# Performance work log

Measured on AMD Instinct MI355X. Metric: run time of the kernel, lower is better.

The kernel has to match this reference:

```python
import jax, jax.numpy as jnp
import numpy as np

QUANT_LEVELS = jnp.array([-1.5, -0.5, 0.5, 1.5], dtype=jnp.float32)
EPS = 1e-5


def setup_inputs() -> dict:
    key = jax.random.key(0)
    k1, k2, k3 = jax.random.split(key, 3)
    B, S, D_IN, D_OUT = 4, 2048, 4096, 4096
    x = jax.random.normal(k1, (B, S, D_IN), dtype=jnp.float32)
    weight_2bit = jax.random.randint(k2, (D_OUT, D_IN), 0, 4, dtype=jnp.int32)
    weight_scale = jnp.ones((1,), dtype=jnp.float32)
    bias = jax.random.normal(k3, (D_OUT,), dtype=jnp.float32)
    return {"x": x, "weight_2bit": weight_2bit, "weight_scale": weight_scale, "bias": bias}


def reference(x, weight_2bit, weight_scale, bias):
    # per-row (last-dim) absmax activation normalization
    x_abs_max = jnp.clip(jnp.max(jnp.abs(x), axis=-1, keepdims=True), EPS)  # [B,S,1]
    x_norm = x / x_abs_max
    # dequantize 2-bit codes to {-1.5,-0.5,0.5,1.5}
    weight_float = QUANT_LEVELS[weight_2bit]  # [D_out, D_in]
    # F.linear: x_norm @ W^T
    out = jnp.einsum('bsd,od->bso', x_norm, weight_float)
    out = out * (x_abs_max * weight_scale)
    out = out + bias
    return out
```

## Files before the change

### kernel.cpp

```cpp
#include <hip/hip_runtime.h>
#include <hip/hip_bf16.h>

typedef __attribute__((ext_vector_type(4))) int i32x4;

#define GLOAD16(gp, lp)                                                        \
  __builtin_amdgcn_global_load_lds(                                            \
      (const __attribute__((address_space(1))) unsigned int*)(const void*)(gp),\
      (__attribute__((address_space(3))) unsigned int*)(void*)(lp), 16, 0, 0)

#define LGKM(n) asm volatile("s_waitcnt lgkmcnt(" #n ")" ::: "memory")
#define VMCNT(n) asm volatile("s_waitcnt vmcnt(" #n ")" ::: "memory")
#define BAR() __builtin_amdgcn_s_barrier()


__global__ void quant_x_i8(const float* __restrict__ x,
                           signed char* __restrict__ xq,
                           float* __restrict__ amax, int K) {
  const int row = blockIdx.x;
  const float* xr = x + (long)row * K;
  const int tid = threadIdx.x;
  const int nv4 = K >> 2;
  float m = 0.f;
  for (int j = tid; j < nv4; j += blockDim.x) {
    float4 v = ((const float4*)xr)[j];
    m = fmaxf(m, fmaxf(fmaxf(fabsf(v.x), fabsf(v.y)),
                       fmaxf(fabsf(v.z), fabsf(v.w))));
  }
  for (int off = 32; off; off >>= 1) m = fmaxf(m, __shfl_xor(m, off));
  __shared__ float red[16];
  const int wid = tid >> 6, lane = tid & 63;
  const int nw = blockDim.x >> 6;
  if (lane == 0) red[wid] = m;
  __syncthreads();
  m = red[0];
  for (int w = 1; w < nw; ++w) m = fmaxf(m, red[w]);
  m = fmaxf(m, 1e-5f);
  if (tid == 0) amax[row] = m;
  const float s = 127.0f / m;
  signed char* xqr = xq + (long)row * K;
  for (int j = tid; j < nv4; j += blockDim.x) {
    float4 v = ((const float4*)xr)[j];
    union { signed char c[4]; int i; } u;
    u.c[0] = (signed char)__float2int_rn(v.x * s);
    u.c[1] = (signed char)__float2int_rn(v.y * s);
    u.c[2] = (signed char)__float2int_rn(v.z * s);
    u.c[3] = (signed char)__float2int_rn(v.w * s);
    ((int*)xqr)[j] = u.i;
  }
}

__global__ void cvt_w_i8(const int* __restrict__ codes,
                         signed char* __restrict__ w8, long n16) {
  long stride = (long)gridDim.x * blockDim.x;
  for (long i = (long)blockIdx.x * blockDim.x + threadIdx.x; i < n16; i += stride) {
    const int4* p = (const int4*)(codes + i * 16);
    int4 a = p[0], b = p[1], c = p[2], d = p[3];
    union { signed char ch[16]; int4 v; } u;
    u.ch[0] = (signed char)(2 * a.x - 3);  u.ch[1] = (signed char)(2 * a.y - 3);
    u.ch[2] = (signed char)(2 * a.z - 3);  u.ch[3] = (signed char)(2 * a.w - 3);
    u.ch[4] = (signed char)(2 * b.x - 3);  u.ch[5] = (signed char)(2 * b.y - 3);
    u.ch[6] = (signed char)(2 * b.z - 3);  u.ch[7] = (signed char)(2 * b.w - 3);
    u.ch[8] = (signed char)(2 * c.x - 3);  u.ch[9] = (signed char)(2 * c.y - 3);
    u.ch[10] = (signed char)(2 * c.z - 3); u.ch[11] = (signed char)(2 * c.w - 3);
    u.ch[12] = (signed char)(2 * d.x - 3); u.ch[13] = (signed char)(2 * d.y - 3);
    u.ch[14] = (signed char)(2 * d.z - 3); u.ch[15] = (signed char)(2 * d.w - 3);
    *(int4*)(w8 + i * 16) = u.v;
  }
}


template <int MIH>
__device__ __forceinline__ void rdA8(const signed char* Asb, i32x4 (&a)[4][2],
                                     int arow, int ccol) {
#pragma unroll
  for (int m4 = 0; m4 < 4; ++m4)
#pragma unroll
    for (int kk = 0; kk < 2; ++kk)
      a[m4][kk] = *(const i32x4*)(Asb + MIH * 16384 + m4 * 2048 + arow +
                                  (ccol ^ (kk << 6)));
}

template <int NIH>
__device__ __forceinline__ void rdB8(const signed char* Bsb, i32x4 (&b)[4][2],
                                     int brw, int ccol) {
#pragma unroll
  for (int n2 = 0; n2 < 2; ++n2)
#pragma unroll
    for (int kk = 0; kk < 2; ++kk)
      b[NIH * 2 + n2][kk] = *(const i32x4*)(Bsb + NIH * 16384 + n2 * 2048 +
                                            brw + (ccol ^ (kk << 6)));
}

template <int MH, int NH>
__device__ __forceinline__ void quad8(i32x4 (&acc)[8][4], const i32x4 (&a)[4][2],
                                      const i32x4 (&b)[4][2]) {
#pragma unroll
  for (int m4 = 0; m4 < 4; ++m4)
#pragma unroll
    for (int n2 = 0; n2 < 2; ++n2)
#pragma unroll
      for (int kk = 0; kk < 2; ++kk)
        acc[MH * 4 + m4][NH * 2 + n2] = __builtin_amdgcn_mfma_i32_16x16x64_i8(
            a[m4][kk], b[NH * 2 + n2][kk], acc[MH * 4 + m4][NH * 2 + n2], 0, 0, 0);
}

__global__ void __launch_bounds__(512, 2) gemm256_i8(
    const signed char* __restrict__ A, const signed char* __restrict__ B,
    const float* __restrict__ amax, const float* __restrict__ bias,
    const float* __restrict__ scalep, float* __restrict__ C, int M, int N,
    int K) {
  extern __shared__ signed char lds[];
  signed char* As0 = lds;
  signed char* As1 = lds + 32768;
  signed char* Bs0 = lds + 65536;
  signed char* Bs1 = lds + 98304;

  const int tid = threadIdx.x;
  const int lane = tid & 63;
  const int wid = tid >> 6;
  const int wr = wid >> 2;
  const int wc = wid & 3;
  const int l15 = lane & 15;
  const int l7 = lane & 7;
  const int lq = lane >> 4;

  const int NT = K >> 7;
  const int nbx = N >> 8;
  const int nwg = gridDim.x;
  const int bid = blockIdx.x;
  const int swz = ((nwg & 7) == 0) ? ((bid & 7) * (nwg >> 3) + (bid >> 3)) : bid;
  const int bx = swz % nbx;
  const int by = swz / nbx;
  const long brow = (long)by << 8;
  const long bcol = (long)bx << 8;

  const signed char* Ag = A + brow * K;
  const signed char* Bg = B + bcol * K;

  const int srl0 = tid >> 3;
  const int scol = ((lane & 7) ^ (lane >> 3)) << 4;
  const int ccol = (lq ^ l7) << 4;
  const int arow = wr * 8192 + l15 * 128;
  const int brw = wc * 4096 + l15 * 128;

  auto stA = [&](signed char* dst, int h, int kt) {
    if (kt >= NT) return;
    const long k0 = ((long)kt << 7) + scol;
#pragma unroll
    for (int r = 0; r < 2; ++r) {
      const int srl = srl0 + (r << 6);
      const int ar = ((srl >> 6) << 7) + (h << 6) + (srl & 63);
      GLOAD16(Ag + (long)ar * K + k0, dst + (h << 14) + (r << 13) + (wid << 10));
    }
  };
  auto stB = [&](signed char* dst, int h, int kt) {
    if (kt >= NT) return;
    const long k0 = ((long)kt << 7) + scol;
#pragma unroll
    for (int r = 0; r < 2; ++r) {
      const int srl = srl0 + (r << 6);
      const int br = ((srl >> 5) << 6) + (((h << 1) + ((srl >> 4) & 1)) << 4) +
                     (srl & 15);
      GLOAD16(Bg + (long)br * K + k0, dst + (h << 14) + (r << 13) + (wid << 10));
    }
  };

  stA(As0, 0, 0); stB(Bs0, 0, 0); stB(Bs0, 1, 0); stA(As0, 1, 0);
  stA(As1, 0, 1); stB(Bs1, 0, 1); stB(Bs1, 1, 1);
  VMCNT(6);
  BAR();

  i32x4 a[4][2], b[4][2];
  i32x4 acc[8][4] = {};

  const int NI = NT >> 1;
  for (int i = 0; i < NI; ++i) {
    const int T = i << 1;
    rdA8<0>(As0, a, arow, ccol);
    rdB8<0>(Bs0, b, brw, ccol);
    stA(As1, 1, T + 1);
    LGKM(8);
    BAR(); LGKM(0);
    __builtin_amdgcn_s_setprio(1); quad8<0, 0>(acc, a, b); __builtin_amdgcn_s_setprio(0);
    BAR();
    rdB8<1>(Bs0, b, brw, ccol);
    stA(As0, 0, T + 2);
    BAR(); LGKM(0);
    __builtin_amdgcn_s_setprio(1); quad8<0, 1>(acc, a, b); __builtin_amdgcn_s_setprio(0);
    BAR();
    rdA8<1>(As0, a, arow, ccol);
    stB(Bs0, 0, T + 2);
    BAR(); LGKM(0);
    __builtin_amdgcn_s_setprio(1); quad8<1, 0>(acc, a, b); __builtin_amdgcn_s_setprio(0);
    BAR();
    stB(Bs0, 1, T + 2);
    BAR();
    __builtin_amdgcn_s_setprio(1); quad8<1, 1>(acc, a, b); __builtin_amdgcn_s_setprio(0);
    if (T + 4 <= NT) { VMCNT(6); } else { VMCNT(0); }
    BAR();
    rdA8<0>(As1, a, arow, ccol);
    rdB8<0>(Bs1, b, brw, ccol);
    stA(As0, 1, T + 2);
    LGKM(8);
    BAR(); LGKM(0);
    __builtin_amdgcn_s_setprio(1); quad8<0, 0>(acc, a, b); __builtin_amdgcn_s_setprio(0);
    BAR();
    rdB8<1>(Bs1, b, brw, ccol);
    stA(As1, 0, T + 3);
    BAR(); LGKM(0);
    __builtin_amdgcn_s_setprio(1); quad8<0, 1>(acc, a, b); __builtin_amdgcn_s_setprio(0);
    BAR();
    rdA8<1>(As1, a, arow, ccol);
    stB(Bs1, 0, T + 3);
    BAR(); LGKM(0);
    __builtin_amdgcn_s_setprio(1); quad8<1, 0>(acc, a, b); __builtin_amdgcn_s_setprio(0);
    BAR();
    stB(Bs1, 1, T + 3);
    BAR();
    __builtin_amdgcn_s_setprio(1); quad8<1, 1>(acc, a, b); __builtin_amdgcn_s_setprio(0);
    if (i + 1 < NI) { VMCNT(6); } else { VMCNT(0); }
    BAR();
  }

  const float ws = scalep[0] * (1.0f / 254.0f);
#pragma unroll
  for (int mi = 0; mi < 8; ++mi) {
    const long row0 = brow + wr * 128 + mi * 16 + lq * 4;
    float am[4];
#pragma unroll
    for (int r = 0; r < 4; ++r) am[r] = amax[row0 + r] * ws;
#pragma unroll
    for (int ni = 0; ni < 4; ++ni) {
      const long col = bcol + wc * 64 + ni * 16 + l15;
      const float bv = bias[col];
#pragma unroll
      for (int r = 0; r < 4; ++r)
        C[(row0 + r) * (long)N + col] = (float)acc[mi][ni][r] * am[r] + bv;
    }
  }
}


__global__ void naive_gemm(const float* __restrict__ x, const int* __restrict__ w2,
                           const float* __restrict__ scalep,
                           const float* __restrict__ bias, float* __restrict__ out,
                           long M, int N, int K) {
  long idx = (long)blockIdx.x * blockDim.x + threadIdx.x;
  if (idx >= M * (long)N) return;
  long m = idx / N;
  int n = (int)(idx % N);
  const float* xr = x + m * (long)K;
  const int* wr = w2 + (long)n * K;
  float s = 0.f;
  for (int k = 0; k < K; ++k) s += xr[k] * ((float)wr[k] - 1.5f);
  out[idx] = s * scalep[0] + bias[n];
}


extern "C" void kernel_launch(void* const* d_in, const int* in_sizes, int n_in,
                              void* d_out, int out_size, void* d_ws, size_t ws_size,
                              hipStream_t stream) {
  const float* x = (const float*)d_in[0];
  const int* w2 = (const int*)d_in[1];
  const float* wscale = (const float*)d_in[2];
  const float* bias = (const float*)d_in[3];
  float* out = (float*)d_out;

  const long xn = (long)in_sizes[0];
  const long wn = (long)in_sizes[1];
  const int N = in_sizes[3];
  const int K = (int)(wn / N);
  const long M = xn / K;

  const size_t need = (size_t)xn + (size_t)wn + (size_t)M * 4;
  const bool fast = (ws_size >= need) && (M % 256 == 0) && (N % 256 == 0) &&
                    (K % 128 == 0) && (wn % 16 == 0);

  if (fast) {
    signed char* xq = (signed char*)d_ws;
    signed char* w8 = (signed char*)d_ws + xn;
    float* amax = (float*)((signed char*)d_ws + xn + wn);

    quant_x_i8<<<(int)M, 256, 0, stream>>>(x, xq, amax, K);
    cvt_w_i8<<<2048, 256, 0, stream>>>(w2, w8, wn / 16);

    hipFuncSetAttribute((const void*)gemm256_i8,
                        hipFuncAttributeMaxDynamicSharedMemorySize, 131072);
    const int grid = (int)((M / 256) * (N / 256));
    gemm256_i8<<<grid, 512, 131072, stream>>>(xq, w8, amax, bias, wscale, out,
                                              (int)M, N, K);
  } else {
    const long total = M * (long)N;
    const int blocks = (int)((total + 255) / 256);
    naive_gemm<<<blocks, 256, 0, stream>>>(x, w2, wscale, bias, out, M, N, K);
  }
}
```

Before: 187.3 us.

## Switch int8 GEMM to 32x32x32 MFMA and merge prep kernels

Replaces the 16x16x64 int8 MFMA tiling with 32x32x32 int8 MFMA instructions. This changes the LDS read pattern, the accumulator layout (i32x16) and the epilogue row mapping. It also merges the activation-quantize and weight-convert kernels into one launch, split by block index. The larger MFMA tiles are meant to cut LDS reads per MAC and raise matrix-core efficiency, while the merged prep removes one launch and lets the two prep jobs run concurrently. The risks are the different throughput of the new instruction and possible LDS bank conflicts from the new read swizzle.

```diff
diff --git a/kernel.cpp b/kernel.cpp
--- a/kernel.cpp
+++ b/kernel.cpp
@@ -2,6 +2,7 @@
 #include <hip/hip_bf16.h>
 
 typedef __attribute__((ext_vector_type(4))) int i32x4;
+typedef __attribute__((ext_vector_type(16))) int i32x16;
 
 #define GLOAD16(gp, lp)                                                        \
   __builtin_amdgcn_global_load_lds(                                            \
@@ -13,95 +14,94 @@
 #define BAR() __builtin_amdgcn_s_barrier()
 
 
-__global__ void quant_x_i8(const float* __restrict__ x,
-                           signed char* __restrict__ xq,
-                           float* __restrict__ amax, int K) {
-  const int row = blockIdx.x;
-  const float* xr = x + (long)row * K;
+__global__ void prep_i8(const float* __restrict__ x,
+                        const int* __restrict__ codes,
+                        signed char* __restrict__ xq,
+                        signed char* __restrict__ w8,
+                        float* __restrict__ amax, int K, int M, long n16) {
+  __shared__ float red[16];
   const int tid = threadIdx.x;
-  const int nv4 = K >> 2;
-  float m = 0.f;
-  for (int j = tid; j < nv4; j += blockDim.x) {
-    float4 v = ((const float4*)xr)[j];
-    m = fmaxf(m, fmaxf(fmaxf(fabsf(v.x), fabsf(v.y)),
-                       fmaxf(fabsf(v.z), fabsf(v.w))));
+  if ((int)blockIdx.x < M) {
+    const int row = blockIdx.x;
+    const float* xr = x + (long)row * K;
+    const int nv4 = K >> 2;
+    float m = 0.f;
+    for (int j = tid; j < nv4; j += blockDim.x) {
+      float4 v = ((const float4*)xr)[j];
+      m = fmaxf(m, fmaxf(fmaxf(fabsf(v.x), fabsf(v.y)),
+                         fmaxf(fabsf(v.z), fabsf(v.w))));
+    }
+    for (int off = 32; off; off >>= 1) m = fmaxf(m, __shfl_xor(m, off));
+    const int wid = tid >> 6, lane = tid & 63;
+    const int nw = blockDim.x >> 6;
+    if (lane == 0) red[wid] = m;
+    __syncthreads();
+    m = red[0];
+    for (int w = 1; w < nw; ++w) m = fmaxf(m, red[w]);
+    m = fmaxf(m, 1e-5f);
+    if (tid == 0) amax[row] = m;
+    const float s = 127.0f / m;
+    signed char* xqr = xq + (long)row * K;
+    for (int j = tid; j < nv4; j += blockDim.x) {
+      float4 v = ((const float4*)xr)[j];
+      union { signed char c[4]; int i; } u;
+      u.c[0] = (signed char)__float2int_rn(v.x * s);
+      u.c[1] = (signed char)__float2int_rn(v.y * s);
+      u.c[2] = (signed char)__float2int_rn(v.z * s);
+      u.c[3] = (signed char)__float2int_rn(v.w * s);
+      ((int*)xqr)[j] = u.i;
+    }
+  } else {
+    const long stride = (long)(gridDim.x - M) * blockDim.x;
+    for (long i = (long)(blockIdx.x - M) * blockDim.x + tid; i < n16;
+         i += stride) {
+      const int4* p = (const int4*)(codes + i * 16);
+      int4 a = p[0], b = p[1], c = p[2], d = p[3];
+      union { signed char ch[16]; int4 v; } u;
+      u.ch[0] = (signed char)(2 * a.x - 3);  u.ch[1] = (signed char)(2 * a.y - 3);
+      u.ch[2] = (signed char)(2 * a.z - 3);  u.ch[3] = (signed char)(2 * a.w - 3);
+      u.ch[4] = (signed char)(2 * b.x - 3);  u.ch[5] = (signed char)(2 * b.y - 3);
+      u.ch[6] = (signed char)(2 * b.z - 3);  u.ch[7] = (signed char)(2 * b.w - 3);
+      u.ch[8] = (signed char)(2 * c.x - 3);  u.ch[9] = (signed char)(2 * c.y - 3);
+      u.ch[10] = (signed char)(2 * c.z - 3); u.ch[11] = (signed char)(2 * c.w - 3);
+      u.ch[12] = (signed char)(2 * d.x - 3); u.ch[13] = (signed char)(2 * d.y - 3);
+      u.ch[14] = (signed char)(2 * d.z - 3); u.ch[15] = (signed char)(2 * d.w - 3);
+      *(int4*)(w8 + i * 16) = u.v;
+    }
   }
-  for (int off = 32; off; off >>= 1) m = fmaxf(m, __shfl_xor(m, off));
-  __shared__ float red[16];
-  const int wid = tid >> 6, lane = tid & 63;
-  const int nw = blockDim.x >> 6;
-  if (lane == 0) red[wid] = m;
-  __syncthreads();
-  m = red[0];
-  for (int w = 1; w < nw; ++w) m = fmaxf(m, red[w]);
-  m = fmaxf(m, 1e-5f);
-  if (tid == 0) amax[row] = m;
-  const float s = 127.0f / m;
-  signed char* xqr = xq + (long)row * K;
-  for (int j = tid; j < nv4; j += blockDim.x) {
-    float4 v = ((const float4*)xr)[j];
-    union { signed char c[4]; int i; } u;
-    u.c[0] = (signed char)__float2int_rn(v.x * s);
-    u.c[1] = (signed char)__float2int_rn(v.y * s);
-    u.c[2] = (signed char)__float2int_rn(v.z * s);
-    u.c[3] = (signed char)__float2int_rn(v.w * s);
-    ((int*)xqr)[j] = u.i;
-  }
-}
-
-__global__ void cvt_w_i8(const int* __restrict__ codes,
-                         signed char* __restrict__ w8, long n16) {
-  long stride = (long)gridDim.x * blockDim.x;
-  for (long i = (long)blockIdx.x * blockDim.x + threadIdx.x; i < n16; i += stride) {
-    const int4* p = (const int4*)(codes + i * 16);
-    int4 a = p[0], b = p[1], c = p[2], d = p[3];
-    union { signed char ch[16]; int4 v; } u;
-    u.ch[0] = (signed char)(2 * a.x - 3);  u.ch[1] = (signed char)(2 * a.y - 3);
-    u.ch[2] = (signed char)(2 * a.z - 3);  u.ch[3] = (signed char)(2 * a.w - 3);
-    u.ch[4] = (signed char)(2 * b.x - 3);  u.ch[5] = (signed char)(2 * b.y - 3);
-    u.ch[6] = (signed char)(2 * b.z - 3);  u.ch[7] = (signed char)(2 * b.w - 3);
-    u.ch[8] = (signed char)(2 * c.x - 3);  u.ch[9] = (signed char)(2 * c.y - 3);
-    u.ch[10] = (signed char)(2 * c.z - 3); u.ch[11] = (signed char)(2 * c.w - 3);
-    u.ch[12] = (signed char)(2 * d.x - 3); u.ch[13] = (signed char)(2 * d.y - 3);
-    u.ch[14] = (signed char)(2 * d.z - 3); u.ch[15] = (signed char)(2 * d.w - 3);
-    *(int4*)(w8 + i * 16) = u.v;
-  }
-}
-
-
-template <int MIH>
-__device__ __forceinline__ void rdA8(const signed char* Asb, i32x4 (&a)[4][2],
-                                     int arow, int ccol) {
-#pragma unroll
-  for (int m4 = 0; m4 < 4; ++m4)
-#pragma unroll
-    for (int kk = 0; kk < 2; ++kk)
-      a[m4][kk] = *(const i32x4*)(Asb + MIH * 16384 + m4 * 2048 + arow +
-                                  (ccol ^ (kk << 6)));
-}
-
-template <int NIH>
-__device__ __forceinline__ void rdB8(const signed char* Bsb, i32x4 (&b)[4][2],
-                                     int brw, int ccol) {
-#pragma unroll
-  for (int n2 = 0; n2 < 2; ++n2)
-#pragma unroll
-    for (int kk = 0; kk < 2; ++kk)
-      b[NIH * 2 + n2][kk] = *(const i32x4*)(Bsb + NIH * 16384 + n2 * 2048 +
-                                            brw + (ccol ^ (kk << 6)));
-}
-
-template <int MH, int NH>
-__device__ __forceinline__ void quad8(i32x4 (&acc)[8][4], const i32x4 (&a)[4][2],
-                                      const i32x4 (&b)[4][2]) {
-#pragma unroll
-  for (int m4 = 0; m4 < 4; ++m4)
-#pragma unroll
-    for (int n2 = 0; n2 < 2; ++n2)
-#pragma unroll
-      for (int kk = 0; kk < 2; ++kk)
-        acc[MH * 4 + m4][NH * 2 + n2] = __builtin_amdgcn_mfma_i32_16x16x64_i8(
-            a[m4][kk], b[NH * 2 + n2][kk], acc[MH * 4 + m4][NH * 2 + n2], 0, 0, 0);
+}
+
+
+template <int MH>
+__device__ __forceinline__ void rdA32(const signed char* Asb, i32x4 (&a)[2][4],
+                                      int abase, int c0) {
+#pragma unroll
+  for (int mb2 = 0; mb2 < 2; ++mb2)
+#pragma unroll
+    for (int kk = 0; kk < 4; ++kk)
+      a[mb2][kk] = *(const i32x4*)(Asb + MH * 16384 + abase + mb2 * 4096 +
+                                   ((((kk << 1) ^ c0)) << 4));
+}
+
+template <int NB>
+__device__ __forceinline__ void rdB32(const signed char* Bsb, i32x4 (&b)[2][4],
+                                      int bbase, int c0) {
+#pragma unroll
+  for (int kk = 0; kk < 4; ++kk)
+    b[NB][kk] = *(const i32x4*)(Bsb + NB * 16384 + bbase +
+                                ((((kk << 1) ^ c0)) << 4));
+}
+
+template <int MH, int NB>
+__device__ __forceinline__ void quad32(i32x16 (&acc)[4][2],
+                                       const i32x4 (&a)[2][4],
+                                       const i32x4 (&b)[2][4]) {
+#pragma unroll
+  for (int mb2 = 0; mb2 < 2; ++mb2)
+#pragma unroll
+    for (int kk = 0; kk < 4; ++kk)
+      acc[MH * 2 + mb2][NB] = __builtin_amdgcn_mfma_i32_32x32x32_i8(
+          a[mb2][kk], b[NB][kk], acc[MH * 2 + mb2][NB], 0, 0, 0);
 }
 
 __global__ void __launch_bounds__(512, 2) gemm256_i8(
@@ -120,9 +120,9 @@
   const int wid = tid >> 6;
   const int wr = wid >> 2;
   const int wc = wid & 3;
-  const int l15 = lane & 15;
+  const int l31 = lane & 31;
   const int l7 = lane & 7;
-  const int lq = lane >> 4;
+  const int lhi = lane >> 5;
 
   const int NT = K >> 7;
   const int nbx = N >> 8;
@@ -139,9 +139,9 @@
 
   const int srl0 = tid >> 3;
   const int scol = ((lane & 7) ^ (lane >> 3)) << 4;
-  const int ccol = (lq ^ l7) << 4;
-  const int arow = wr * 8192 + l15 * 128;
-  const int brw = wc * 4096 + l15 * 128;
+  const int c0 = lhi ^ l7;
+  const int abase = (wr * 64 + l31) * 128;
+  const int bbase = (wc * 32 + l31) * 128;
 
   auto stA = [&](signed char* dst, int h, int kt) {
     if (kt >= NT) return;
@@ -170,72 +170,75 @@
   VMCNT(6);
   BAR();
 
-  i32x4 a[4][2], b[4][2];
-  i32x4 acc[8][4] = {};
+  i32x4 a[2][4], b[2][4];
+  i32x16 acc[4][2] = {};
 
   const int NI = NT >> 1;
   for (int i = 0; i < NI; ++i) {
     const int T = i << 1;
-    rdA8<0>(As0, a, arow, ccol);
-    rdB8<0>(Bs0, b, brw, ccol);
+    rdA32<0>(As0, a, abase, c0);
+    rdB32<0>(Bs0, b, bbase, c0);
     stA(As1, 1, T + 1);
     LGKM(8);
     BAR(); LGKM(0);
-    __builtin_amdgcn_s_setprio(1); quad8<0, 0>(acc, a, b); __builtin_amdgcn_s_setprio(0);
-    BAR();
-    rdB8<1>(Bs0, b, brw, ccol);
+    __builtin_amdgcn_s_setprio(1); quad32<0, 0>(acc, a, b); __builtin_amdgcn_s_setprio(0);
+    BAR();
+    rdB32<1>(Bs0, b, bbase, c0);
     stA(As0, 0, T + 2);
     BAR(); LGKM(0);
-    __builtin_amdgcn_s_setprio(1); quad8<0, 1>(acc, a, b); __builtin_amdgcn_s_setprio(0);
-    BAR();
-    rdA8<1>(As0, a, arow, ccol);
+    __builtin_amdgcn_s_setprio(1); quad32<0, 1>(acc, a, b); __builtin_amdgcn_s_setprio(0);
+    BAR();
+    rdA32<1>(As0, a, abase, c0);
     stB(Bs0, 0, T + 2);
     BAR(); LGKM(0);
-    __builtin_amdgcn_s_setprio(1); quad8<1, 0>(acc, a, b); __builtin_amdgcn_s_setprio(0);
+    __builtin_amdgcn_s_setprio(1); quad32<1, 0>(acc, a, b); __builtin_amdgcn_s_setprio(0);
     BAR();
     stB(Bs0, 1, T + 2);
     BAR();
-    __builtin_amdgcn_s_setprio(1); quad8<1, 1>(acc, a, b); __builtin_amdgcn_s_setprio(0);
+    __builtin_amdgcn_s_setprio(1); quad32<1, 1>(acc, a, b); __builtin_amdgcn_s_setprio(0);
     if (T + 4 <= NT) { VMCNT(6); } else { VMCNT(0); }
     BAR();
-    rdA8<0>(As1, a, arow, ccol);
-    rdB8<0>(Bs1, b, brw, ccol);
+    rdA32<0>(As1, a, abase, c0);
+    rdB32<0>(Bs1, b, bbase, c0);
     stA(As0, 1, T + 2);
     LGKM(8);
     BAR(); LGKM(0);
-    __builtin_amdgcn_s_setprio(1); quad8<0, 0>(acc, a, b); __builtin_amdgcn_s_setprio(0);
-    BAR();
-    rdB8<1>(Bs1, b, brw, ccol);
+    __builtin_amdgcn_s_setprio(1); quad32<0, 0>(acc, a, b); __builtin_amdgcn_s_setprio(0);
+    BAR();
+    rdB32<1>(Bs1, b, bbase, c0);
     stA(As1, 0, T + 3);
     BAR(); LGKM(0);
-    __builtin_amdgcn_s_setprio(1); quad8<0, 1>(acc, a, b); __builtin_amdgcn_s_setprio(0);
-    BAR();
-    rdA8<1>(As1, a, arow, ccol);
+    __builtin_amdgcn_s_setprio(1); quad32<0, 1>(acc, a, b); __builtin_amdgcn_s_setprio(0);
+    BAR();
+    rdA32<1>(As1, a, abase, c0);
     stB(Bs1, 0, T + 3);
     BAR(); LGKM(0);
-    __builtin_amdgcn_s_setprio(1); quad8<1, 0>(acc, a, b); __builtin_amdgcn_s_setprio(0);
+    __builtin_amdgcn_s_setprio(1); quad32<1, 0>(acc, a, b); __builtin_amdgcn_s_setprio(0);
     BAR();
     stB(Bs1, 1, T + 3);
     BAR();
-    __builtin_amdgcn_s_setprio(1); quad8<1, 1>(acc, a, b); __builtin_amdgcn_s_setprio(0);
+    __builtin_amdgcn_s_setprio(1); quad32<1, 1>(acc, a, b); __builtin_amdgcn_s_setprio(0);
     if (i + 1 < NI) { VMCNT(6); } else { VMCNT(0); }
     BAR();
   }
 
   const float ws = scalep[0] * (1.0f / 254.0f);
 #pragma unroll
-  for (int mi = 0; mi < 8; ++mi) {
-    const long row0 = brow + wr * 128 + mi * 16 + lq * 4;
-    float am[4];
-#pragma unroll
-    for (int r = 0; r < 4; ++r) am[r] = amax[row0 + r] * ws;
-#pragma unroll
-    for (int ni = 0; ni < 4; ++ni) {
-      const long col = bcol + wc * 64 + ni * 16 + l15;
+  for (int mb = 0; mb < 4; ++mb) {
+    const long rowb = brow + wr * 128 + mb * 32 + 4 * lhi;
+    float am[16];
+#pragma unroll
+    for (int reg = 0; reg < 16; ++reg)
+      am[reg] = amax[rowb + (reg & 3) + 8 * (reg >> 2)] * ws;
+#pragma unroll
+    for (int nb = 0; nb < 2; ++nb) {
+      const long col = bcol + wc * 64 + nb * 32 + l31;
       const float bv = bias[col];
 #pragma unroll
-      for (int r = 0; r < 4; ++r)
-        C[(row0 + r) * (long)N + col] = (float)acc[mi][ni][r] * am[r] + bv;
+      for (int reg = 0; reg < 16; ++reg) {
+        const long row = rowb + (reg & 3) + 8 * (reg >> 2);
+        C[row * (long)N + col] = (float)acc[mb][nb][reg] * am[reg] + bv;
+      }
     }
   }
 }
@@ -281,8 +284,8 @@
     signed char* w8 = (signed char*)d_ws + xn;
     float* amax = (float*)((signed char*)d_ws + xn + wn);
 
-    quant_x_i8<<<(int)M, 256, 0, stream>>>(x, xq, amax, K);
-    cvt_w_i8<<<2048, 256, 0, stream>>>(w2, w8, wn / 16);
+    prep_i8<<<(int)M + 2048, 256, 0, stream>>>(x, w2, xq, w8, amax, K, (int)M,
+                                               wn / 16);
 
     hipFuncSetAttribute((const void*)gemm256_i8,
                         hipFuncAttributeMaxDynamicSharedMemorySize, 131072);
```

Result: slower. 201.9 us (+7.8%).

## Fuse activation and weight prep kernels; restructure LDS fragment reads in GEMM

Applied to the files above, without the earlier changes.

Merges the activation absmax quantization and the weight code conversion into one launch, with block ranges split by blockIdx, to remove a kernel launch and let both prep jobs run concurrently. In the int8 GEMM main loop it adds a second A fragment register set and issues both B half-reads up front, so LDS reads overlap more MFMA work and lgkmcnt waits are relaxed. The cost is more registers, which may lower occupancy or spill, and the fast-path condition is tightened to K divisible by 256.

```diff
diff --git a/kernel.cpp b/kernel.cpp
--- a/kernel.cpp
+++ b/kernel.cpp
@@ -13,58 +13,60 @@
 #define BAR() __builtin_amdgcn_s_barrier()
 
 
-__global__ void quant_x_i8(const float* __restrict__ x,
-                           signed char* __restrict__ xq,
-                           float* __restrict__ amax, int K) {
-  const int row = blockIdx.x;
-  const float* xr = x + (long)row * K;
+__global__ void prep_i8(const float* __restrict__ x,
+                        const int* __restrict__ codes,
+                        signed char* __restrict__ xq,
+                        signed char* __restrict__ w8,
+                        float* __restrict__ amax, int K, int M, long n16) {
+  __shared__ float red[16];
   const int tid = threadIdx.x;
-  const int nv4 = K >> 2;
-  float m = 0.f;
-  for (int j = tid; j < nv4; j += blockDim.x) {
-    float4 v = ((const float4*)xr)[j];
-    m = fmaxf(m, fmaxf(fmaxf(fabsf(v.x), fabsf(v.y)),
-                       fmaxf(fabsf(v.z), fabsf(v.w))));
-  }
-  for (int off = 32; off; off >>= 1) m = fmaxf(m, __shfl_xor(m, off));
-  __shared__ float red[16];
-  const int wid = tid >> 6, lane = tid & 63;
-  const int nw = blockDim.x >> 6;
-  if (lane == 0) red[wid] = m;
-  __syncthreads();
-  m = red[0];
-  for (int w = 1; w < nw; ++w) m = fmaxf(m, red[w]);
-  m = fmaxf(m, 1e-5f);
-  if (tid == 0) amax[row] = m;
-  const float s = 127.0f / m;
-  signed char* xqr = xq + (long)row * K;
-  for (int j = tid; j < nv4; j += blockDim.x) {
-    float4 v = ((const float4*)xr)[j];
-    union { signed char c[4]; int i; } u;
-    u.c[0] = (signed char)__float2int_rn(v.x * s);
-    u.c[1] = (signed char)__float2int_rn(v.y * s);
-    u.c[2] = (signed char)__float2int_rn(v.z * s);
-    u.c[3] = (signed char)__float2int_rn(v.w * s);
-    ((int*)xqr)[j] = u.i;
-  }
-}
-
-__global__ void cvt_w_i8(const int* __restrict__ codes,
-                         signed char* __restrict__ w8, long n16) {
-  long stride = (long)gridDim.x * blockDim.x;
-  for (long i = (long)blockIdx.x * blockDim.x + threadIdx.x; i < n16; i += stride) {
-    const int4* p = (const int4*)(codes + i * 16);
-    int4 a = p[0], b = p[1], c = p[2], d = p[3];
-    union { signed char ch[16]; int4 v; } u;
-    u.ch[0] = (signed char)(2 * a.x - 3);  u.ch[1] = (signed char)(2 * a.y - 3);
-    u.ch[2] = (signed char)(2 * a.z - 3);  u.ch[3] = (signed char)(2 * a.w - 3);
-    u.ch[4] = (signed char)(2 * b.x - 3);  u.ch[5] = (signed char)(2 * b.y - 3);
-    u.ch[6] = (signed char)(2 * b.z - 3);  u.ch[7] = (signed char)(2 * b.w - 3);
-    u.ch[8] = (signed char)(2 * c.x - 3);  u.ch[9] = (signed char)(2 * c.y - 3);
-    u.ch[10] = (signed char)(2 * c.z - 3); u.ch[11] = (signed char)(2 * c.w - 3);
-    u.ch[12] = (signed char)(2 * d.x - 3); u.ch[13] = (signed char)(2 * d.y - 3);
-    u.ch[14] = (signed char)(2 * d.z - 3); u.ch[15] = (signed char)(2 * d.w - 3);
-    *(int4*)(w8 + i * 16) = u.v;
+  if ((int)blockIdx.x < M) {
+    const int row = blockIdx.x;
+    const float* xr = x + (long)row * K;
+    const int nv4 = K >> 2;
+    float m = 0.f;
+    for (int j = tid; j < nv4; j += blockDim.x) {
+      float4 v = ((const float4*)xr)[j];
+      m = fmaxf(m, fmaxf(fmaxf(fabsf(v.x), fabsf(v.y)),
+                         fmaxf(fabsf(v.z), fabsf(v.w))));
+    }
+    for (int off = 32; off; off >>= 1) m = fmaxf(m, __shfl_xor(m, off));
+    const int wid = tid >> 6, lane = tid & 63;
+    const int nw = blockDim.x >> 6;
+    if (lane == 0) red[wid] = m;
+    __syncthreads();
+    m = red[0];
+    for (int w = 1; w < nw; ++w) m = fmaxf(m, red[w]);
+    m = fmaxf(m, 1e-5f);
+    if (tid == 0) amax[row] = m;
+    const float s = 127.0f / m;
+    signed char* xqr = xq + (long)row * K;
+    for (int j = tid; j < nv4; j += blockDim.x) {
+      float4 v = ((const float4*)xr)[j];
+      union { signed char c[4]; int i; } u;
+      u.c[0] = (signed char)__float2int_rn(v.x * s);
+      u.c[1] = (signed char)__float2int_rn(v.y * s);
+      u.c[2] = (signed char)__float2int_rn(v.z * s);
+      u.c[3] = (signed char)__float2int_rn(v.w * s);
+      ((int*)xqr)[j] = u.i;
+    }
+  } else {
+    const long stride = (long)(gridDim.x - M) * blockDim.x;
+    for (long i = (long)(blockIdx.x - M) * blockDim.x + tid; i < n16;
+         i += stride) {
+      const int4* p = (const int4*)(codes + i * 16);
+      int4 a = p[0], b = p[1], c = p[2], d = p[3];
+      union { signed char ch[16]; int4 v; } u;
+      u.ch[0] = (signed char)(2 * a.x - 3);  u.ch[1] = (signed char)(2 * a.y - 3);
+      u.ch[2] = (signed char)(2 * a.z - 3);  u.ch[3] = (signed char)(2 * a.w - 3);
+      u.ch[4] = (signed char)(2 * b.x - 3);  u.ch[5] = (signed char)(2 * b.y - 3);
+      u.ch[6] = (signed char)(2 * b.z - 3);  u.ch[7] = (signed char)(2 * b.w - 3);
+      u.ch[8] = (signed char)(2 * c.x - 3);  u.ch[9] = (signed char)(2 * c.y - 3);
+      u.ch[10] = (signed char)(2 * c.z - 3); u.ch[11] = (signed char)(2 * c.w - 3);
+      u.ch[12] = (signed char)(2 * d.x - 3); u.ch[13] = (signed char)(2 * d.y - 3);
+      u.ch[14] = (signed char)(2 * d.z - 3); u.ch[15] = (signed char)(2 * d.w - 3);
+      *(int4*)(w8 + i * 16) = u.v;
+    }
   }
 }
 
@@ -170,54 +172,54 @@
   VMCNT(6);
   BAR();
 
-  i32x4 a[4][2], b[4][2];
+  i32x4 a1[4][2], a2[4][2], b[4][2];
   i32x4 acc[8][4] = {};
 
   const int NI = NT >> 1;
   for (int i = 0; i < NI; ++i) {
     const int T = i << 1;
-    rdA8<0>(As0, a, arow, ccol);
+    rdA8<0>(As0, a1, arow, ccol);
     rdB8<0>(Bs0, b, brw, ccol);
+    rdB8<1>(Bs0, b, brw, ccol);
     stA(As1, 1, T + 1);
     LGKM(8);
-    BAR(); LGKM(0);
-    __builtin_amdgcn_s_setprio(1); quad8<0, 0>(acc, a, b); __builtin_amdgcn_s_setprio(0);
-    BAR();
-    rdB8<1>(Bs0, b, brw, ccol);
+    BAR(); LGKM(4);
+    __builtin_amdgcn_s_setprio(1); quad8<0, 0>(acc, a1, b); __builtin_amdgcn_s_setprio(0);
+    BAR();
+    rdA8<1>(As0, a2, arow, ccol);
     stA(As0, 0, T + 2);
-    BAR(); LGKM(0);
-    __builtin_amdgcn_s_setprio(1); quad8<0, 1>(acc, a, b); __builtin_amdgcn_s_setprio(0);
-    BAR();
-    rdA8<1>(As0, a, arow, ccol);
+    BAR(); LGKM(8);
+    __builtin_amdgcn_s_setprio(1); quad8<0, 1>(acc, a1, b); __builtin_amdgcn_s_setprio(0);
+    BAR();
     stB(Bs0, 0, T + 2);
     BAR(); LGKM(0);
-    __builtin_amdgcn_s_setprio(1); quad8<1, 0>(acc, a, b); __builtin_amdgcn_s_setprio(0);
+    __builtin_amdgcn_s_setprio(1); quad8<1, 0>(acc, a2, b); __builtin_amdgcn_s_setprio(0);
     BAR();
     stB(Bs0, 1, T + 2);
     BAR();
-    __builtin_amdgcn_s_setprio(1); quad8<1, 1>(acc, a, b); __builtin_amdgcn_s_setprio(0);
+    __builtin_amdgcn_s_setprio(1); quad8<1, 1>(acc, a2, b); __builtin_amdgcn_s_setprio(0);
     if (T + 4 <= NT) { VMCNT(6); } else { VMCNT(0); }
     BAR();
-    rdA8<0>(As1, a, arow, ccol);
+    rdA8<0>(As1, a1, arow, ccol);
     rdB8<0>(Bs1, b, brw, ccol);
+    rdB8<1>(Bs1, b, brw, ccol);
     stA(As0, 1, T + 2);
     LGKM(8);
-    BAR(); LGKM(0);
-    __builtin_amdgcn_s_setprio(1); quad8<0, 0>(acc, a, b); __builtin_amdgcn_s_setprio(0);
-    BAR();
-    rdB8<1>(Bs1, b, brw, ccol);
+    BAR(); LGKM(4);
+    __builtin_amdgcn_s_setprio(1); quad8<0, 0>(acc, a1, b); __builtin_amdgcn_s_setprio(0);
+    BAR();
+    rdA8<1>(As1, a2, arow, ccol);
     stA(As1, 0, T + 3);
-    BAR(); LGKM(0);
-    __builtin_amdgcn_s_setprio(1); quad8<0, 1>(acc, a, b); __builtin_amdgcn_s_setprio(0);
-    BAR();
-    rdA8<1>(As1, a, arow, ccol);
+    BAR(); LGKM(8);
+    __builtin_amdgcn_s_setprio(1); quad8<0, 1>(acc, a1, b); __builtin_amdgcn_s_setprio(0);
+    BAR();
     stB(Bs1, 0, T + 3);
     BAR(); LGKM(0);
-    __builtin_amdgcn_s_setprio(1); quad8<1, 0>(acc, a, b); __builtin_amdgcn_s_setprio(0);
+    __builtin_amdgcn_s_setprio(1); quad8<1, 0>(acc, a2, b); __builtin_amdgcn_s_setprio(0);
     BAR();
     stB(Bs1, 1, T + 3);
     BAR();
-    __builtin_amdgcn_s_setprio(1); quad8<1, 1>(acc, a, b); __builtin_amdgcn_s_setprio(0);
+    __builtin_amdgcn_s_setprio(1); quad8<1, 1>(acc, a2, b); __builtin_amdgcn_s_setprio(0);
     if (i + 1 < NI) { VMCNT(6); } else { VMCNT(0); }
     BAR();
   }
@@ -274,15 +276,15 @@
 
   const size_t need = (size_t)xn + (size_t)wn + (size_t)M * 4;
   const bool fast = (ws_size >= need) && (M % 256 == 0) && (N % 256 == 0) &&
-                    (K % 128 == 0) && (wn % 16 == 0);
+                    (K % 256 == 0) && (wn % 16 == 0);
 
   if (fast) {
     signed char* xq = (signed char*)d_ws;
     signed char* w8 = (signed char*)d_ws + xn;
     float* amax = (float*)((signed char*)d_ws + xn + wn);
 
-    quant_x_i8<<<(int)M, 256, 0, stream>>>(x, xq, amax, K);
-    cvt_w_i8<<<2048, 256, 0, stream>>>(w2, w8, wn / 16);
+    prep_i8<<<(int)M + 2048, 256, 0, stream>>>(x, w2, xq, w8, amax, K, (int)M,
+                                               wn / 16);
 
     hipFuncSetAttribute((const void*)gemm256_i8,
                         hipFuncAttributeMaxDynamicSharedMemorySize, 131072);
```

New measurement: 239.5 us. 27.8% more time.
